# Performance work log

Hardware: AMD Instinct MI355X
Metric: run time of the kernel (lower is better)

The kernel has to match this reference:

```python
import jax, jax.numpy as jnp
import numpy as np

HEADS = 16
GROUPS = 4


def setup_inputs() -> dict:
    key = jax.random.key(0)
    k1, k2, k3, k4 = jax.random.split(key, 4)
    d_model = 2048
    d_kv = d_model * GROUPS // HEADS  # 512
    x = jax.random.normal(k1, (2, 2048, d_model), dtype=jnp.float32)
    Wq = jax.random.normal(k2, (d_model, d_model), dtype=jnp.float32) * (d_model ** -0.5)
    Wk = jax.random.normal(k3, (d_kv, d_model), dtype=jnp.float32) * (d_model ** -0.5)
    Wv = jax.random.normal(k4, (d_kv, d_model), dtype=jnp.float32) * (d_model ** -0.5)
    return {"x": x, "Wq": Wq, "Wk": Wk, "Wv": Wv}


def reference(x, Wq, Wk, Wv):
    b, t, c = x.shape
    hd = c // HEADS  # head dim
    h2g = HEADS // GROUPS  # query heads per kv group
    # projections (nn.Linear applies x @ W.T)
    q = (x @ Wq.T).reshape(b, t, HEADS, hd).transpose(0, 2, 1, 3)   # [b,H,t,hd]
    k = (x @ Wk.T).reshape(b, t, GROUPS, hd).transpose(0, 2, 1, 3)  # [b,G,t,hd]
    v = (x @ Wv.T).reshape(b, t, GROUPS, hd).transpose(0, 2, 1, 3)  # [b,G,t,hd]
    # GQA broadcast: group query heads by kv group
    qg = q.reshape(b, GROUPS, h2g, t, hd)                            # [b,G,h2g,t,hd]
    scores = jnp.einsum('bghqd,bgkd->bghqk', qg, k) * (hd ** -0.5)  # [b,G,h2g,t,t]
    causal = jnp.tril(jnp.ones((t, t), dtype=bool))
    scores = jnp.where(causal, scores, -jnp.inf)
    weights = jax.nn.softmax(scores, axis=-1)
    out = jnp.einsum('bghqk,bgkd->bghqd', weights, v)               # [b,G,h2g,t,hd]
    out = out.reshape(b, HEADS, t, hd).transpose(0, 2, 1, 3).reshape(b, t, c)
    return out
```

## Files before the change

kernel.cpp:

```cpp
#include <hip/hip_runtime.h>
#include <hip/hip_bf16.h>

typedef __bf16 bf16x8 __attribute__((ext_vector_type(8)));
typedef float f32x4 __attribute__((ext_vector_type(4)));

#define MFMA16(a,b,c) __builtin_amdgcn_mfma_f32_16x16x32_bf16(a,b,c,0,0,0)
#define GLL16(src, dst) __builtin_amdgcn_global_load_lds( \
    (const __attribute__((address_space(1))) unsigned int*)(src), \
    (__attribute__((address_space(3))) unsigned int*)(dst), 16, 0, 0)

__device__ inline unsigned int pack_bf16(float a, float b) {
    unsigned short ua = __builtin_bit_cast(unsigned short, (__bf16)a);
    unsigned short ub = __builtin_bit_cast(unsigned short, (__bf16)b);
    return ((unsigned int)ub << 16) | ua;
}
__device__ inline short bf_s(float v) {
    __bf16 b = (__bf16)v;
    return __builtin_bit_cast(short, b);
}

__global__ void cvt_all(const float* __restrict__ x,  const float* __restrict__ wq,
                        const float* __restrict__ wk, const float* __restrict__ wv,
                        __bf16* __restrict__ xb, __bf16* __restrict__ wb) {
    long i = (long)(blockIdx.x * blockDim.x + threadIdx.x) * 8;
    const float* src; __bf16* dst;
    if (i < 8388608)       { src = x  + i;              dst = xb + i; }
    else if (i < 12582912) { src = wq + (i - 8388608);  dst = wb + (i - 8388608); }
    else if (i < 13631488) { src = wk + (i - 12582912); dst = wb + (i - 12582912 + 4194304); }
    else                   { src = wv + (i - 13631488); dst = wb + (i - 13631488 + 5242880); }
    float4 a = *(const float4*)src;
    float4 b = *(const float4*)(src + 4);
    bf16x8 r;
    r[0] = (__bf16)a.x; r[1] = (__bf16)a.y; r[2] = (__bf16)a.z; r[3] = (__bf16)a.w;
    r[4] = (__bf16)b.x; r[5] = (__bf16)b.y; r[6] = (__bf16)b.z; r[7] = (__bf16)b.w;
    *(bf16x8*)dst = r;
}

__global__ __launch_bounds__(256) void gemm_qkv(const __bf16* __restrict__ A,
                                                const __bf16* __restrict__ B,
                                                __bf16* __restrict__ Qb,
                                                __bf16* __restrict__ Kf,
                                                __bf16* __restrict__ Vf,
                                                float qscale) {
    const int K = 2048;
    __shared__ __bf16 As[2 * 4096];
    __shared__ __bf16 Bs[2 * 4096];

    int tid = threadIdx.x;
    int wave = tid >> 6, lane = tid & 63;
    int quad = lane >> 4, l16 = lane & 15;

    int tm = blockIdx.x & 31, tn = blockIdx.x >> 5;

    const __bf16* Abase = A + (size_t)tm * 128 * K + (size_t)l16 * K + quad * 8;
    const __bf16* Bbase = B + (size_t)tn * 128 * K + (size_t)l16 * K + quad * 8;

    f32x4 acc[4][4] = {};

    auto stage = [&](int kt, int buf) {
#pragma unroll
        for (int rr = 0; rr < 2; ++rr) {
            int fb = rr * 4 + wave;
            GLL16(Abase + (size_t)fb * 16 * K + kt, As + buf * 4096 + fb * 512 + lane * 8);
            GLL16(Bbase + (size_t)fb * 16 * K + kt, Bs + buf * 4096 + fb * 512 + lane * 8);
        }
    };

    const int nk = K >> 5;
    stage(0, 0);
    for (int it = 0; it < nk; ++it) {
        __syncthreads();
        if (it + 1 < nk) stage((it + 1) << 5, (it + 1) & 1);
        const __bf16* Ab = As + (it & 1) * 4096;
        const __bf16* Bb = Bs + (it & 1) * 4096;
        bf16x8 af[4], bfr[4];
#pragma unroll
        for (int i = 0; i < 4; ++i)
            af[i] = *(const bf16x8*)(Ab + ((wave >> 1) * 4 + i) * 512 + lane * 8);
#pragma unroll
        for (int j = 0; j < 4; ++j)
            bfr[j] = *(const bf16x8*)(Bb + ((wave & 1) * 4 + j) * 512 + lane * 8);
#pragma unroll
        for (int i = 0; i < 4; ++i)
#pragma unroll
            for (int j = 0; j < 4; ++j)
                acc[i][j] = MFMA16(af[i], bfr[j], acc[i][j]);
    }

    int colbase = tn * 128 + (wave & 1) * 64;
#pragma unroll
    for (int i = 0; i < 4; ++i) {
        int row0 = tm * 128 + (wave >> 1) * 64 + i * 16 + quad * 4;
        int b = row0 >> 11, tok0 = row0 & 2047;
#pragma unroll
        for (int j = 0; j < 4; ++j) {
            int col = colbase + j * 16 + l16;
            if (tn < 16) {
#pragma unroll
                for (int r = 0; r < 4; ++r)
                    Qb[(size_t)(row0 + r) * 2048 + col] = (__bf16)(acc[i][j][r] * qscale);
            } else if (tn < 20) {
                int d_all = col - 2048;
                int g = d_all >> 7, dd = d_all & 127;
                int dt = dd >> 5, q4 = (dd >> 3) & 3, jj = dd & 7;
                int tb = tok0 >> 4, tl0 = tok0 & 15;
                __bf16* base = Kf + ((((size_t)(b * 4 + g) * 128 + tb) * 4 + dt) * 512)
                               + (q4 * 16 + tl0) * 8 + jj;
#pragma unroll
                for (int r = 0; r < 4; ++r)
                    base[r * 8] = (__bf16)acc[i][j][r];
            } else {
                int d_all = col - 2560;
                int g = d_all >> 7, dd = d_all & 127;
                int nto = dd >> 4, dl = dd & 15;
                int ch = tok0 >> 6, kk = (tok0 >> 5) & 1;
                int q4v = (tok0 >> 3) & 3, jv0 = tok0 & 7;
                size_t off = ((((size_t)(b * 4 + g) * 32 + ch) * 16) + nto * 2 + kk) * 512
                             + (q4v * 16 + dl) * 8 + jv0;
                short4 pk;
                pk.x = bf_s(acc[i][j][0]); pk.y = bf_s(acc[i][j][1]);
                pk.z = bf_s(acc[i][j][2]); pk.w = bf_s(acc[i][j][3]);
                *(short4*)(Vf + off) = pk;
            }
        }
    }
}

__global__ __launch_bounds__(256) void attn_mfma(const __bf16* __restrict__ Q,
                                                 const __bf16* __restrict__ Kf,
                                                 const __bf16* __restrict__ Vf,
                                                 float* __restrict__ O) {
    const int T = 2048, CM = 2048, HD = 128;
    __shared__ __bf16 Ks[8192];
    __shared__ __bf16 Vs[8192];
    __shared__ __bf16 Pl[8192];

    int tid = threadIdx.x;
    int wave = tid >> 6, lane = tid & 63;
    int quad = lane >> 4, l16 = lane & 15;

    int bg = blockIdx.x & 7;
    int slot = blockIdx.x >> 3;
    int qb = (slot < 32) ? (63 - slot) : (slot - 32);
    int b = bg >> 2, g = bg & 3;
    int h = g * 4 + wave;
    int q0 = qb * 32;

    bf16x8 qf[2][4];
    const __bf16* qbase = Q + (size_t)b * T * CM + (size_t)h * HD;
#pragma unroll
    for (int nt = 0; nt < 2; ++nt)
#pragma unroll
        for (int dt = 0; dt < 4; ++dt)
            qf[nt][dt] = *(const bf16x8*)(qbase + (size_t)(q0 + nt * 16 + l16) * CM
                                          + dt * 32 + quad * 8);

    const __bf16* kcb = Kf + (size_t)(b * 4 + g) * 262144;
    const __bf16* vcb = Vf + (size_t)(b * 4 + g) * 262144;

    float m_r[2] = {-1e30f, -1e30f}, l_r[2] = {0.f, 0.f};
    f32x4 o_acc[2][8] = {};
    __bf16* Pw = Pl + wave * 2048;

    int nch = (qb >> 1) + 1;
    for (int ch = 0; ch < nch; ++ch) {
        __syncthreads();
        {
            const __bf16* kg = kcb + ch * 8192 + wave * 2048 + lane * 8;
            const __bf16* vg = vcb + ch * 8192 + wave * 2048 + lane * 8;
            __bf16* kl = Ks + wave * 2048 + lane * 8;
            __bf16* vl = Vs + wave * 2048 + lane * 8;
#pragma unroll
            for (int i = 0; i < 4; ++i) GLL16(kg + i * 512, kl + i * 512);
#pragma unroll
            for (int i = 0; i < 4; ++i) GLL16(vg + i * 512, vl + i * 512);
        }
        __syncthreads();

        f32x4 st[2][4] = {};
#pragma unroll
        for (int t = 0; t < 4; ++t)
#pragma unroll
            for (int dt = 0; dt < 4; ++dt) {
                bf16x8 kfv = *(const bf16x8*)(Ks + (t * 4 + dt) * 512 + lane * 8);
                st[0][t] = MFMA16(kfv, qf[0][dt], st[0][t]);
                st[1][t] = MFMA16(kfv, qf[1][dt], st[1][t]);
            }

        bool diag = (ch == nch - 1);
        float alpha[2];
#pragma unroll
        for (int nt = 0; nt < 2; ++nt) {
            if (diag) {
                int qg = q0 + nt * 16 + l16;
#pragma unroll
                for (int t = 0; t < 4; ++t)
#pragma unroll
                    for (int r = 0; r < 4; ++r)
                        if (ch * 64 + t * 16 + quad * 4 + r > qg) st[nt][t][r] = -1e30f;
            }
            float cmax = -1e30f;
#pragma unroll
            for (int t = 0; t < 4; ++t)
                cmax = fmaxf(cmax, fmaxf(fmaxf(st[nt][t][0], st[nt][t][1]),
                                         fmaxf(st[nt][t][2], st[nt][t][3])));
            cmax = fmaxf(cmax, __shfl_xor(cmax, 16));
            cmax = fmaxf(cmax, __shfl_xor(cmax, 32));
            float mnew = fmaxf(m_r[nt], cmax);
            alpha[nt] = __expf(m_r[nt] - mnew);
            m_r[nt] = mnew;
            float ps = 0.f;
#pragma unroll
            for (int t = 0; t < 4; ++t) {
                float p0 = __expf(st[nt][t][0] - mnew);
                float p1 = __expf(st[nt][t][1] - mnew);
                float p2 = __expf(st[nt][t][2] - mnew);
                float p3 = __expf(st[nt][t][3] - mnew);
                ps += (p0 + p1) + (p2 + p3);
                int off = (nt * 2 + (t >> 1)) * 512 + ((t & 1) * 2 + (quad >> 1)) * 128
                          + l16 * 8 + (quad & 1) * 4;
                unsigned long long pk =
                    (unsigned long long)pack_bf16(p0, p1) |
                    ((unsigned long long)pack_bf16(p2, p3) << 32);
                *(unsigned long long*)(Pw + off) = pk;
            }
            ps += __shfl_xor(ps, 16);
            ps += __shfl_xor(ps, 32);
            l_r[nt] = l_r[nt] * alpha[nt] + ps;
        }

#pragma unroll
        for (int mt = 0; mt < 2; ++mt)
#pragma unroll
            for (int r = 0; r < 4; ++r) {
                float alr = __shfl(alpha[mt], quad * 4 + r);
#pragma unroll
                for (int nto = 0; nto < 8; ++nto)
                    o_acc[mt][nto][r] *= alr;
            }

#pragma unroll
        for (int mt = 0; mt < 2; ++mt)
#pragma unroll
            for (int kk = 0; kk < 2; ++kk) {
                bf16x8 pf = *(const bf16x8*)(Pw + (mt * 2 + kk) * 512 + lane * 8);
#pragma unroll
                for (int nto = 0; nto < 8; ++nto) {
                    bf16x8 vf = *(const bf16x8*)(Vs + (nto * 2 + kk) * 512 + lane * 8);
                    o_acc[mt][nto] = MFMA16(pf, vf, o_acc[mt][nto]);
                }
            }
    }

    float* obase = O + (size_t)b * T * CM + (size_t)h * HD;
#pragma unroll
    for (int mt = 0; mt < 2; ++mt) {
        float invl = 1.f / l_r[mt];
#pragma unroll
        for (int r = 0; r < 4; ++r) {
            float ir = __shfl(invl, quad * 4 + r);
            float* orow = obase + (size_t)(q0 + 16 * mt + quad * 4 + r) * CM;
#pragma unroll
            for (int nto = 0; nto < 8; ++nto)
                orow[nto * 16 + l16] = o_acc[mt][nto][r] * ir;
        }
    }
}

extern "C" void kernel_launch(void* const* d_in, const int* in_sizes, int n_in,
                              void* d_out, int out_size, void* d_ws, size_t ws_size,
                              hipStream_t stream) {
    const float* x  = (const float*)d_in[0];
    const float* Wq = (const float*)d_in[1];
    const float* Wk = (const float*)d_in[2];
    const float* Wv = (const float*)d_in[3];
    float* out = (float*)d_out;

    const float qscale = 0.08838834764831845f;

    __bf16* xb = (__bf16*)d_ws;
    __bf16* Wb = xb + 8388608;
    __bf16* Qb = Wb + 6291456;
    __bf16* Kfr = Qb + 8388608;
    __bf16* Vfr = Kfr + 2097152;

    cvt_all<<<7168, 256, 0, stream>>>(x, Wq, Wk, Wv, xb, Wb);
    gemm_qkv<<<768, 256, 0, stream>>>(xb, Wb, Qb, Kfr, Vfr, qscale);
    attn_mfma<<<512, 256, 0, stream>>>(Qb, Kfr, Vfr, out);
}
```

Baseline: 278.7 us.

## Triple-buffer QKV GEMM and double-buffer K/V chunks in attention

```diff
diff --git a/kernel.cpp b/kernel.cpp
--- a/kernel.cpp
+++ b/kernel.cpp
@@ -43,8 +43,8 @@
                                                 __bf16* __restrict__ Vf,
                                                 float qscale) {
     const int K = 2048;
-    __shared__ __bf16 As[2 * 4096];
-    __shared__ __bf16 Bs[2 * 4096];
+    __shared__ __bf16 As[3 * 4096];
+    __shared__ __bf16 Bs[3 * 4096];
 
     int tid = threadIdx.x;
     int wave = tid >> 6, lane = tid & 63;
@@ -68,11 +68,15 @@
 
     const int nk = K >> 5;
     stage(0, 0);
+    stage(32, 1);
+    asm volatile("s_waitcnt vmcnt(4)" ::: "memory");
+    __builtin_amdgcn_s_barrier();
+
+    int sl = 0, s2 = 2;
     for (int it = 0; it < nk; ++it) {
-        __syncthreads();
-        if (it + 1 < nk) stage((it + 1) << 5, (it + 1) & 1);
-        const __bf16* Ab = As + (it & 1) * 4096;
-        const __bf16* Bb = Bs + (it & 1) * 4096;
+        if (it + 2 < nk) stage((it + 2) << 5, s2);
+        const __bf16* Ab = As + sl * 4096;
+        const __bf16* Bb = Bs + sl * 4096;
         bf16x8 af[4], bfr[4];
 #pragma unroll
         for (int i = 0; i < 4; ++i)
@@ -85,6 +89,13 @@
 #pragma unroll
             for (int j = 0; j < 4; ++j)
                 acc[i][j] = MFMA16(af[i], bfr[j], acc[i][j]);
+        if (it + 1 < nk) {
+            if (it + 2 < nk) asm volatile("s_waitcnt vmcnt(4)" ::: "memory");
+            else             asm volatile("s_waitcnt vmcnt(0)" ::: "memory");
+            __builtin_amdgcn_s_barrier();
+        }
+        sl = (sl == 2) ? 0 : sl + 1;
+        s2 = (s2 == 2) ? 0 : s2 + 1;
     }
 
     int colbase = tn * 128 + (wave & 1) * 64;
@@ -131,8 +142,8 @@
                                                  const __bf16* __restrict__ Vf,
                                                  float* __restrict__ O) {
     const int T = 2048, CM = 2048, HD = 128;
-    __shared__ __bf16 Ks[8192];
-    __shared__ __bf16 Vs[8192];
+    __shared__ __bf16 Ks[2 * 8192];
+    __shared__ __bf16 Vs[2 * 8192];
     __shared__ __bf16 Pl[8192];
 
     int tid = threadIdx.x;
@@ -162,27 +173,38 @@
     f32x4 o_acc[2][8] = {};
     __bf16* Pw = Pl + wave * 2048;
 
+    auto stage_kv = [&](int ch, int buf) {
+        const __bf16* kg = kcb + ch * 8192 + wave * 2048 + lane * 8;
+        const __bf16* vg = vcb + ch * 8192 + wave * 2048 + lane * 8;
+        __bf16* kl = Ks + buf * 8192 + wave * 2048 + lane * 8;
+        __bf16* vl = Vs + buf * 8192 + wave * 2048 + lane * 8;
+#pragma unroll
+        for (int i = 0; i < 4; ++i) GLL16(kg + i * 512, kl + i * 512);
+#pragma unroll
+        for (int i = 0; i < 4; ++i) GLL16(vg + i * 512, vl + i * 512);
+    };
+
     int nch = (qb >> 1) + 1;
+    stage_kv(0, 0);
     for (int ch = 0; ch < nch; ++ch) {
-        __syncthreads();
-        {
-            const __bf16* kg = kcb + ch * 8192 + wave * 2048 + lane * 8;
-            const __bf16* vg = vcb + ch * 8192 + wave * 2048 + lane * 8;
-            __bf16* kl = Ks + wave * 2048 + lane * 8;
-            __bf16* vl = Vs + wave * 2048 + lane * 8;
-#pragma unroll
-            for (int i = 0; i < 4; ++i) GLL16(kg + i * 512, kl + i * 512);
-#pragma unroll
-            for (int i = 0; i < 4; ++i) GLL16(vg + i * 512, vl + i * 512);
-        }
-        __syncthreads();
+        __builtin_amdgcn_s_barrier();
+        if (ch + 1 < nch) {
+            stage_kv(ch + 1, (ch + 1) & 1);
+            asm volatile("s_waitcnt vmcnt(8)" ::: "memory");
+        } else {
+            asm volatile("s_waitcnt vmcnt(0)" ::: "memory");
+        }
+        __builtin_amdgcn_s_barrier();
+
+        const __bf16* Kb = Ks + (ch & 1) * 8192;
+        const __bf16* Vb = Vs + (ch & 1) * 8192;
 
         f32x4 st[2][4] = {};
 #pragma unroll
         for (int t = 0; t < 4; ++t)
 #pragma unroll
             for (int dt = 0; dt < 4; ++dt) {
-                bf16x8 kfv = *(const bf16x8*)(Ks + (t * 4 + dt) * 512 + lane * 8);
+                bf16x8 kfv = *(const bf16x8*)(Kb + (t * 4 + dt) * 512 + lane * 8);
                 st[0][t] = MFMA16(kfv, qf[0][dt], st[0][t]);
                 st[1][t] = MFMA16(kfv, qf[1][dt], st[1][t]);
             }
@@ -246,7 +268,7 @@
                 bf16x8 pf = *(const bf16x8*)(Pw + (mt * 2 + kk) * 512 + lane * 8);
 #pragma unroll
                 for (int nto = 0; nto < 8; ++nto) {
-                    bf16x8 vf = *(const bf16x8*)(Vs + (nto * 2 + kk) * 512 + lane * 8);
+                    bf16x8 vf = *(const bf16x8*)(Vb + (nto * 2 + kk) * 512 + lane * 8);
                     o_acc[mt][nto] = MFMA16(pf, vf, o_acc[mt][nto]);
                 }
             }
```

Result: no change. 280.3 us (+0.6%).
